# Kernel optimization log

Hardware: AMD Instinct MI355X
Metric: run time of the kernel (lower is better)

Reference implementation:

```python
import jax, jax.numpy as jnp
import numpy as np

B, N, D, H = 4, 2048, 768, 12
HD = D // H
SCALE = HD ** -0.5


def setup_inputs() -> dict:
    key = jax.random.key(0)
    k1, k2, k3 = jax.random.split(key, 3)
    x = jax.random.normal(k1, (B, N, D), dtype=jnp.float32)
    w_qkv = jax.random.normal(k2, (D, 3 * D), dtype=jnp.float32) * (D ** -0.5)
    w_proj = jax.random.normal(k3, (D, D), dtype=jnp.float32) * (D ** -0.5)
    b_proj = jnp.zeros((D,), dtype=jnp.float32)
    return {"x": x, "w_qkv": w_qkv, "w_proj": w_proj, "b_proj": b_proj}


def reference(x, w_qkv, w_proj, b_proj):
    b, n, d = x.shape
    qkv = x @ w_qkv                      # [b, n, 3d]
    q, k, v = jnp.split(qkv, 3, axis=-1)
    # [b, n, d] -> [b, h, n, hd]
    split_heads = lambda t: t.reshape(b, n, H, HD).transpose(0, 2, 1, 3)
    q, k, v = split_heads(q), split_heads(k), split_heads(v)
    dots = jnp.einsum('bhqd,bhkd->bhqk', q, k) * SCALE   # [b, h, n, n]
    attn = jax.nn.softmax(dots, axis=-1)
    q_attn = attn[:, :, 0, :]            # attention row of query token 0: [b, h, n]
    # dropout p=0 (eval) -> identity
    out = jnp.einsum('bhqk,bhkd->bhqd', attn, v)          # [b, h, n, hd]
    out = out.transpose(0, 2, 1, 3).reshape(b, n, d)      # [b, n, d]
    return out @ w_proj + b_proj, q_attn
```

## Files before the change

kernel.cpp:

```cpp
#include <hip/hip_runtime.h>


typedef unsigned short u16;
typedef __attribute__((ext_vector_type(8))) short bf8;
typedef __attribute__((ext_vector_type(4))) short bf4;
typedef __attribute__((ext_vector_type(4))) int i4;
typedef __attribute__((ext_vector_type(4))) float f4;

#define MFMA16(a, b, c) __builtin_amdgcn_mfma_f32_16x16x32_bf16((a), (b), (c), 0, 0, 0)

#if __has_builtin(__builtin_amdgcn_exp2f)
#define EXP2(x) __builtin_amdgcn_exp2f(x)
#else
#define EXP2(x) __expf((x) * 0.6931471805599453f)
#endif

__device__ __forceinline__ float b2f(u16 h) {
  union { unsigned u; float f; } v; v.u = ((unsigned)h) << 16; return v.f;
}
__device__ __forceinline__ u16 f2b(float f) {
  union { float f; unsigned u; } v; v.f = f;
  unsigned r = v.u + 0x7fffu + ((v.u >> 16) & 1u);
  return (u16)(r >> 16);
}
__device__ __forceinline__ unsigned pack2(float a, float b) {
#if __has_builtin(__builtin_amdgcn_perm)
  return __builtin_amdgcn_perm(__builtin_bit_cast(unsigned, b),
                               __builtin_bit_cast(unsigned, a), 0x07060302u);
#else
  return (__builtin_bit_cast(unsigned, b) & 0xFFFF0000u) |
         (__builtin_bit_cast(unsigned, a) >> 16);
#endif
}
__device__ __forceinline__ void gload16(const u16* g, u16* l) {
  __builtin_amdgcn_global_load_lds(
      (const __attribute__((address_space(1))) void*)g,
      (__attribute__((address_space(3))) void*)l, 16, 0, 0);
}
__device__ __forceinline__ int detect_f32(const u16* x) {
  unsigned v = x[2 * (threadIdx.x & 63)];
  unsigned e = (v >> 7) & 0xFF;
  return __ballot(e >= 0x8E) != 0ull;
}

__global__ __launch_bounds__(256) void prep(
    const void* __restrict__ x, u16* __restrict__ xbf,
    const void* __restrict__ wqkv, u16* __restrict__ wqkvT,
    const void* __restrict__ wproj, u16* __restrict__ wprojT) {
  const int z = blockIdx.z;
  if (z == 2) {
    const int f32 = detect_f32((const u16*)x);
    const int lin = blockIdx.y * 72 + blockIdx.x;
    if (f32) {
      const float2* in = (const float2*)x;
      unsigned* out = (unsigned*)xbf;
      for (int i = lin * 256 + threadIdx.x; i < 3145728; i += 442368) {
        float2 v = in[i];
        out[i] = (unsigned)f2b(v.x) | ((unsigned)f2b(v.y) << 16);
      }
    } else {
      const unsigned* in = (const unsigned*)x;
      unsigned* out = (unsigned*)xbf;
      for (int i = lin * 256 + threadIdx.x; i < 3145728; i += 442368)
        out[i] = in[i];
    }
    return;
  }
  if (z == 1 && blockIdx.x >= 24) return;
  const void* in = z ? wproj : wqkv;
  u16* out = z ? wprojT : wqkvT;
  const int R = 768, C = z ? 768 : 2304;
  __shared__ u16 tile[32][33];
  const int f32 = detect_f32((const u16*)x);
  const int bx = blockIdx.x * 32, by = blockIdx.y * 32;
  const int tx = threadIdx.x & 31, ty = threadIdx.x >> 5;
#pragma unroll
  for (int i = 0; i < 4; i++) {
    size_t idx = (size_t)(by + ty + i * 8) * C + bx + tx;
    tile[ty + i * 8][tx] = f32 ? f2b(((const float*)in)[idx]) : ((const u16*)in)[idx];
  }
  __syncthreads();
#pragma unroll
  for (int i = 0; i < 4; i++)
    out[(size_t)(bx + ty + i * 8) * R + by + tx] = tile[tx][ty + i * 8];
}

__global__ __launch_bounds__(512, 4) void gemm_qkv8(
    const u16* __restrict__ A, const u16* __restrict__ Bt,
    u16* __restrict__ Cq, u16* __restrict__ Vt) {
  __shared__ alignas(16) u16 L[3][13312];
  const int t = threadIdx.x;
  const int lane = t & 63, wave = t >> 6;
  const int wr = wave >> 1, wc = wave & 1;
  const int quad = lane >> 4, l16 = lane & 15;
  const int bm = blockIdx.y * 128, bn = blockIdx.x * 288;
  const int dcol = ((lane & 3) ^ ((lane >> 3) & 3)) * 8;
  const int swzU = (quad ^ ((l16 >> 1) & 3)) * 8;
  const int drow = lane >> 2;
  f4 acc[2][9] = {};

#define STAGE(kt, buf)                                                       \
  {                                                                          \
    _Pragma("unroll")                                                        \
    for (int s = 0; s < 4; s++) {                                            \
      int c = wave + s * 8;                                                  \
      if (c >= 26) c = wave;            \
      const int isB = c >= 8;                                                \
      const int rb = isB ? c - 8 : c;                                        \
      const u16* src = (isB ? Bt : A) +                                      \
          (size_t)((isB ? bn : bm) + rb * 16 + drow) * 768 +                 \
          (kt) * 32 + dcol;                                                  \
      u16* dst = &L[buf][(isB ? 4096 : 0) + rb * 512];                       \
      gload16(src, dst);                                                     \
    }                                                                        \
  }

  STAGE(0, 0);
  STAGE(1, 1);

  int cur = 0;
  for (int j = 0; j < 24; j++) {
    if (j < 23) {
      asm volatile("s_waitcnt vmcnt(4)" ::: "memory");
    } else {
      asm volatile("s_waitcnt vmcnt(0)" ::: "memory");
    }
    __builtin_amdgcn_s_barrier();
    if (j + 2 < 24) {
      int pre = cur + 2; if (pre >= 3) pre -= 3;
      STAGE(j + 2, pre);
    }
    const u16* Lb = &L[cur][0];
    bf8 af[2];
#pragma unroll
    for (int m = 0; m < 2; m++)
      af[m] = *(const bf8*)&Lb[(wr * 32 + m * 16 + l16) * 32 + swzU];
#pragma unroll
    for (int p = 0; p < 3; p++) {
      bf8 bfr[3];
#pragma unroll
      for (int nn = 0; nn < 3; nn++)
        bfr[nn] = *(const bf8*)&Lb[4096 +
            (wc * 144 + (p * 3 + nn) * 16 + l16) * 32 + swzU];
      __builtin_amdgcn_s_setprio(1);
#pragma unroll
      for (int nn = 0; nn < 3; nn++)
#pragma unroll
        for (int m = 0; m < 2; m++)
          acc[m][p * 3 + nn] = MFMA16(af[m], bfr[nn], acc[m][p * 3 + nn]);
      __builtin_amdgcn_s_setprio(0);
    }
    cur = (cur == 2) ? 0 : cur + 1;
  }
#undef STAGE

  const int b_ = bm >> 11;
#pragma unroll
  for (int m = 0; m < 2; m++) {
    const int row0 = bm + wr * 32 + m * 16 + quad * 4;
    const int n0 = row0 & 2047;
    const int n2 = (n0 & ~31) | (((n0 >> 2) & 3) << 3) | (((n0 >> 4) & 1) << 2);
#pragma unroll
    for (int ni = 0; ni < 9; ni++) {
      const int col = bn + wc * 144 + ni * 16 + l16;
      if (col >= 1536) {
        const int colv = col - 1536, h = colv >> 6, d = colv & 63;
        bf4 pk = {(short)f2b(acc[m][ni][0]), (short)f2b(acc[m][ni][1]),
                  (short)f2b(acc[m][ni][2]), (short)f2b(acc[m][ni][3])};
        *(bf4*)&Vt[(size_t)((b_ * 12 + h) * 64 + d) * 2048 + n2] = pk;
      } else {
#pragma unroll
        for (int r = 0; r < 4; r++)
          Cq[(size_t)(row0 + r) * 2304 + col] = f2b(acc[m][ni][r]);
      }
    }
  }
}

template <int BIAS, int QATTN>
__global__ __launch_bounds__(256, 4) void gemm_bt(
    const u16* __restrict__ A, const u16* __restrict__ Bt,
    const void* __restrict__ bias, void* __restrict__ C,
    int M, int Ncols, int K, const u16* __restrict__ xdet,
    u16* __restrict__ Vt, const float* __restrict__ qe,
    const float* __restrict__ lout) {
  if (QATTN && blockIdx.x == 6) {
    const int f32o = detect_f32(xdet);
    const int base = blockIdx.y * 1536;
    for (int j = threadIdx.x; j < 1536; j += 256) {
      int idx = base + j;
      float v = qe[idx] * (1.f / lout[idx >> 11]);
      size_t oidx = (size_t)6291456 + idx;
      if (f32o) ((float*)C)[oidx] = v; else ((u16*)C)[oidx] = f2b(v);
    }
    return;
  }
  __shared__ alignas(16) u16 Al[2][128 * 32];
  __shared__ alignas(16) u16 Bl[2][128 * 32];
  const int t = threadIdx.x;
  const int lane = t & 63, wave = t >> 6;
  const int wr = wave >> 1, wc = wave & 1;
  const int quad = lane >> 4, l16 = lane & 15;
  const int bm = blockIdx.y * 128, bn = blockIdx.x * 128;
  const int f32o = BIAS ? detect_f32(xdet) : 0;
  const int grow = lane >> 2, gcol = (lane & 3) * 8;
  const int chunk0 = wave * 2, chunk1 = wave * 2 + 1;
  const int arow0 = chunk0 * 16 + grow, arow1 = chunk1 * 16 + grow;
  f4 acc[4][4] = {};
  gload16(A + (size_t)(bm + arow0) * K + gcol, &Al[0][chunk0 * 512]);
  gload16(Bt + (size_t)(bn + arow0) * K + gcol, &Bl[0][chunk0 * 512]);
  gload16(A + (size_t)(bm + arow1) * K + gcol, &Al[0][chunk1 * 512]);
  gload16(Bt + (size_t)(bn + arow1) * K + gcol, &Bl[0][chunk1 * 512]);
  const int NIT = K >> 5;
  for (int i = 0; i < NIT; i++) {
    const int cur = i & 1, nxt = cur ^ 1;
    __syncthreads();
    if (i + 1 < NIT) {
      int k0 = (i + 1) << 5;
      gload16(A + (size_t)(bm + arow0) * K + k0 + gcol, &Al[nxt][chunk0 * 512]);
      gload16(Bt + (size_t)(bn + arow0) * K + k0 + gcol, &Bl[nxt][chunk0 * 512]);
      gload16(A + (size_t)(bm + arow1) * K + k0 + gcol, &Al[nxt][chunk1 * 512]);
      gload16(Bt + (size_t)(bn + arow1) * K + k0 + gcol, &Bl[nxt][chunk1 * 512]);
    }
    bf8 af[4], bfr[4];
#pragma unroll
    for (int mt = 0; mt < 4; mt++)
      af[mt] = *(const bf8*)&Al[cur][(wr * 64 + mt * 16 + l16) * 32 + quad * 8];
#pragma unroll
    for (int nt = 0; nt < 4; nt++)
      bfr[nt] = *(const bf8*)&Bl[cur][(wc * 64 + nt * 16 + l16) * 32 + quad * 8];
#pragma unroll
    for (int mt = 0; mt < 4; mt++)
#pragma unroll
      for (int nt = 0; nt < 4; nt++)
        acc[mt][nt] = MFMA16(af[mt], bfr[nt], acc[mt][nt]);
  }
  if (Vt != nullptr && bn >= 1536) {
    const int b = bm >> 11;
#pragma unroll
    for (int mt = 0; mt < 4; mt++) {
      int n0 = (bm & 2047) + wr * 64 + mt * 16 + quad * 4;
      int n2 = (n0 & ~31) | (((n0 >> 2) & 3) << 3) | (((n0 >> 4) & 1) << 2);
#pragma unroll
      for (int nt = 0; nt < 4; nt++) {
        int colv = bn - 1536 + wc * 64 + nt * 16 + l16;
        int h = colv >> 6, d = colv & 63;
        bf4 pk = {(short)f2b(acc[mt][nt][0]), (short)f2b(acc[mt][nt][1]),
                  (short)f2b(acc[mt][nt][2]), (short)f2b(acc[mt][nt][3])};
        *(bf4*)&Vt[(size_t)((b * 12 + h) * 64 + d) * 2048 + n2] = pk;
      }
    }
    return;
  }
#pragma unroll
  for (int mt = 0; mt < 4; mt++) {
    int row = bm + wr * 64 + mt * 16 + quad * 4;
#pragma unroll
    for (int nt = 0; nt < 4; nt++) {
      int col = bn + wc * 64 + nt * 16 + l16;
      float bv = 0.f;
      if (BIAS)
        bv = f32o ? ((const float*)bias)[col] : b2f(((const u16*)bias)[col]);
#pragma unroll
      for (int r = 0; r < 4; r++) {
        size_t idx = (size_t)(row + r) * Ncols + col;
        float v = acc[mt][nt][r] + bv;
        if (f32o) ((float*)C)[idx] = v; else ((u16*)C)[idx] = f2b(v);
      }
    }
  }
}

__global__ __launch_bounds__(256, 3) void flash_attn(
    const u16* __restrict__ qkv, const u16* __restrict__ Vt,
    u16* __restrict__ O, float* __restrict__ qe, float* __restrict__ lout) {
  __shared__ alignas(16) u16 lds[3][8192];
  const int t = threadIdx.x, lane = t & 63, wave = t >> 6;
  const int quad = lane >> 4, l16 = lane & 15;
  const int id = blockIdx.x;
  const int bh = (id & 7) + 8 * (id >> 7);
  const int qtile = (id >> 3) & 15;
  const int b = bh / 12, h = bh - b * 12;
  const int q0 = qtile * 128 + wave * 32;
  const bool dumpP = (qe != nullptr) && (qtile == 0) && (wave == 0);
  const float SCALE2 = 0.125f * 1.44269504089f;
  const float mM0 = -16.f;
  bf8 qf[2][2];
#pragma unroll
  for (int qt = 0; qt < 2; qt++) {
    const u16* Qr = qkv + (size_t)(b * 2048 + q0 + qt * 16 + l16) * 2304 + h * 64;
    bf8 r0 = *(const bf8*)(Qr + quad * 8);
    bf8 r1 = *(const bf8*)(Qr + 32 + quad * 8);
#pragma unroll
    for (int j = 0; j < 8; j++) {
      qf[qt][0][j] = (short)f2b(b2f((u16)r0[j]) * SCALE2);
      qf[qt][1][j] = (short)f2b(b2f((u16)r1[j]) * SCALE2);
    }
  }
  bf8 ones;
#pragma unroll
  for (int j = 0; j < 8; j++) ones[j] = (short)0x3F80;
  const u16* Kb = qkv + (size_t)(b * 2048) * 2304 + 768 + h * 64;
  const u16* Vb = Vt + (size_t)((b * 12 + h) * 64) * 2048;
  const int drow = wave * 16 + (lane >> 2);
  const int dcol = ((lane & 3) ^ ((lane >> 3) & 3)) * 8;
  const int swz = (quad ^ ((l16 >> 1) & 3)) * 8;
  f4 o[2][4] = {};
  f4 lacc[2] = {};

#define STAGE(tile, buf)                                            \
  {                                                                 \
    int n1_ = (tile) * 64;                                          \
    const u16* Kt_ = Kb + (size_t)(n1_ + drow) * 2304 + dcol;       \
    const u16* Vr_ = Vb + (size_t)drow * 2048 + n1_ + dcol;         \
    u16* base_ = &lds[buf][wave * 512];                             \
    gload16(Kt_, base_);                                            \
    gload16(Kt_ + 32, base_ + 2048);                                \
    gload16(Vr_, base_ + 4096);                                     \
    gload16(Vr_ + 32, base_ + 6144);                                \
  }

  STAGE(0, 0);
  STAGE(1, 1);

  int cur = 0;
  for (int i = 0; i < 32; i++) {
    if (i < 31) {
      asm volatile("s_waitcnt vmcnt(4)" ::: "memory");
    } else {
      asm volatile("s_waitcnt vmcnt(0)" ::: "memory");
    }
    __builtin_amdgcn_s_barrier();
    if (i + 2 < 32) {
      int pre = cur + 2; if (pre >= 3) pre -= 3;
      STAGE(i + 2, pre);
    }
    const u16* K0 = &lds[cur][0];
    const u16* K1 = &lds[cur][2048];
    union { i4 i; bf8 b; } pf[2][2];
#pragma unroll
    for (int kt = 0; kt < 4; kt++) {
      bf8 kf0 = *(const bf8*)&K0[(kt * 16 + l16) * 32 + swz];
      bf8 kf1 = *(const bf8*)&K1[(kt * 16 + l16) * 32 + swz];
#pragma unroll
      for (int qt = 0; qt < 2; qt++) {
        f4 z = {mM0, mM0, mM0, mM0};
        z = MFMA16(kf0, qf[qt][0], z);
        z = MFMA16(kf1, qf[qt][1], z);
        float e0 = EXP2(z[0]);
        float e1 = EXP2(z[1]);
        float e2 = EXP2(z[2]);
        float e3 = EXP2(z[3]);
        if (qt == 0 && dumpP && l16 == 0) {
          f4 ev = {e0, e1, e2, e3};
          *(f4*)&qe[bh * 2048 + i * 64 + kt * 16 + quad * 4] = ev;
        }
        pf[qt][kt >> 1].i[(kt & 1) * 2 + 0] = (int)pack2(e0, e1);
        pf[qt][kt >> 1].i[(kt & 1) * 2 + 1] = (int)pack2(e2, e3);
      }
    }
#pragma unroll
    for (int pair = 0; pair < 2; pair++) {
      const u16* Vp = &lds[cur][4096 + pair * 2048];
      lacc[0] = MFMA16(ones, pf[0][pair].b, lacc[0]);
      lacc[1] = MFMA16(ones, pf[1][pair].b, lacc[1]);
#pragma unroll
      for (int nt = 0; nt < 4; nt++) {
        bf8 vf = *(const bf8*)&Vp[(nt * 16 + l16) * 32 + swz];
        o[0][nt] = MFMA16(vf, pf[0][pair].b, o[0][nt]);
        o[1][nt] = MFMA16(vf, pf[1][pair].b, o[1][nt]);
      }
    }
    cur = (cur == 2) ? 0 : cur + 1;
  }
#undef STAGE
#pragma unroll
  for (int qt = 0; qt < 2; qt++) {
    float l = lacc[qt][0];
    if (qt == 0 && dumpP && lane == 0) lout[bh] = l;
    float inv = 1.f / l;
    size_t row = (size_t)(b * 2048 + q0 + qt * 16 + l16) * 768 + h * 64;
#pragma unroll
    for (int nt = 0; nt < 4; nt++) {
      bf4 pk = {(short)f2b(o[qt][nt][0] * inv), (short)f2b(o[qt][nt][1] * inv),
                (short)f2b(o[qt][nt][2] * inv), (short)f2b(o[qt][nt][3] * inv)};
      *(bf4*)&O[row + nt * 16 + quad * 4] = pk;
    }
  }
}

__global__ __launch_bounds__(256) void qattn_row0(
    const u16* __restrict__ qkv, void* __restrict__ out,
    const u16* __restrict__ xdet) {
  const int bh = blockIdx.x, b = bh / 12, h = bh % 12;
  __shared__ float qs[64];
  __shared__ float sv[2048];
  __shared__ float red[8];
  const int t = threadIdx.x;
  const int f32o = detect_f32(xdet);
  if (t < 64) qs[t] = b2f(qkv[(size_t)(b * 2048) * 2304 + h * 64 + t]);
  __syncthreads();
  float lmax = -1e30f;
  for (int k = t; k < 2048; k += 256) {
    const u16* Kr = qkv + (size_t)(b * 2048 + k) * 2304 + 768 + h * 64;
    float acc = 0.f;
#pragma unroll
    for (int j = 0; j < 8; j++) {
      bf8 kv = *(const bf8*)(Kr + j * 8);
#pragma unroll
      for (int d = 0; d < 8; d++) acc += qs[j * 8 + d] * b2f((u16)kv[d]);
    }
    acc *= 0.125f;
    sv[k] = acc;
    lmax = fmaxf(lmax, acc);
  }
#pragma unroll
  for (int off = 32; off >= 1; off >>= 1) lmax = fmaxf(lmax, __shfl_xor(lmax, off, 64));
  if ((t & 63) == 0) red[t >> 6] = lmax;
  __syncthreads();
  const float bmax = fmaxf(fmaxf(red[0], red[1]), fmaxf(red[2], red[3]));
  float lsum = 0.f;
  for (int k = t; k < 2048; k += 256) {
    float e = __expf(sv[k] - bmax);
    sv[k] = e;
    lsum += e;
  }
#pragma unroll
  for (int off = 32; off >= 1; off >>= 1) lsum += __shfl_xor(lsum, off, 64);
  if ((t & 63) == 0) red[4 + (t >> 6)] = lsum;
  __syncthreads();
  const float inv = 1.f / (red[4] + red[5] + red[6] + red[7]);
  for (int k = t; k < 2048; k += 256) {
    size_t idx = (size_t)6291456 + (size_t)bh * 2048 + k;
    float v = sv[k] * inv;
    if (f32o) ((float*)out)[idx] = v; else ((u16*)out)[idx] = f2b(v);
  }
}

extern "C" void kernel_launch(void* const* d_in, const int* in_sizes, int n_in,
                              void* d_out, int out_size, void* d_ws, size_t ws_size,
                              hipStream_t stream) {
  const void* x_raw      = d_in[0];
  const void* w_qkv_raw  = d_in[1];
  const void* w_proj_raw = d_in[2];
  const void* b_proj_raw = d_in[3];
  const u16* xdet = (const u16*)x_raw;
  char* ws = (char*)d_ws;
  u16* xbf    = (u16*)(ws + 256);
  u16* wqkvT  = (u16*)(ws + 12583168);
  u16* wprojT = (u16*)(ws + 16122112);
  u16* qkv    = (u16*)(ws + 17301760);
  u16* Vt     = (u16*)(ws + 55050496);
  float* qe   = (float*)(ws + 67633408);
  float* lout = (float*)(ws + 68026624);
  u16* attn   = xbf;
  const bool fused = ws_size >= 68026816ull;

  prep<<<dim3(72, 24, 3), 256, 0, stream>>>(
      x_raw, xbf, w_qkv_raw, wqkvT, w_proj_raw, wprojT);
  gemm_qkv8<<<dim3(8, 64), 512, 0, stream>>>(xbf, wqkvT, qkv, Vt);
  flash_attn<<<dim3(768), 256, 0, stream>>>(qkv, Vt, attn,
                                            fused ? qe : nullptr,
                                            fused ? lout : nullptr);
  if (fused) {
    gemm_bt<1, 1><<<dim3(7, 64), 256, 0, stream>>>(
        attn, wprojT, b_proj_raw, d_out, 8192, 768, 768, xdet, nullptr, qe, lout);
  } else {
    gemm_bt<1, 0><<<dim3(6, 64), 256, 0, stream>>>(
        attn, wprojT, b_proj_raw, d_out, 8192, 768, 768, xdet, nullptr, nullptr, nullptr);
    qattn_row0<<<dim3(48), 256, 0, stream>>>(qkv, d_out, xdet);
  }
}
```

Measured before the change: 209.1 us.

## Add dedicated projection GEMM with smaller tiles and triple-buffered async loads

New measurement: 208.2 us. No clear change (-0.4%).

```diff
diff --git a/kernel.cpp b/kernel.cpp
--- a/kernel.cpp
+++ b/kernel.cpp
@@ -172,6 +172,102 @@
 #pragma unroll
         for (int r = 0; r < 4; r++)
           Cq[(size_t)(row0 + r) * 2304 + col] = f2b(acc[m][ni][r]);
+      }
+    }
+  }
+}
+
+__global__ __launch_bounds__(256, 3) void gemm_proj4(
+    const u16* __restrict__ A, const u16* __restrict__ Bt,
+    const void* __restrict__ bias, void* __restrict__ C,
+    const u16* __restrict__ xdet, const float* __restrict__ qe,
+    const float* __restrict__ lout) {
+  if (blockIdx.x == 6) {
+    if (blockIdx.y >= 64) return;
+    const int f32o = detect_f32(xdet);
+    const int base = blockIdx.y * 1536;
+    for (int j = threadIdx.x; j < 1536; j += 256) {
+      int idx = base + j;
+      float v = qe[idx] * (1.f / lout[idx >> 11]);
+      size_t oidx = (size_t)6291456 + idx;
+      if (f32o) ((float*)C)[oidx] = v; else ((u16*)C)[oidx] = f2b(v);
+    }
+    return;
+  }
+  __shared__ alignas(16) u16 L[3][6144];
+  const int t = threadIdx.x;
+  const int lane = t & 63, wave = t >> 6;
+  const int wr = wave >> 1, wc = wave & 1;
+  const int quad = lane >> 4, l16 = lane & 15;
+  const int bm = blockIdx.y * 64, bn = blockIdx.x * 128;
+  const int f32o = detect_f32(xdet);
+  const int dcol = ((lane & 3) ^ ((lane >> 3) & 3)) * 8;
+  const int swzU = (quad ^ ((l16 >> 1) & 3)) * 8;
+  const int drow = lane >> 2;
+  f4 acc[2][4] = {};
+
+#define STAGE(kt, buf)                                                       \
+  {                                                                          \
+    _Pragma("unroll")                                                        \
+    for (int s = 0; s < 3; s++) {                                            \
+      const int c = wave + s * 4;                                            \
+      const int isB = c >= 4;                                                \
+      const int rb = isB ? c - 4 : c;                                        \
+      const u16* src = (isB ? Bt : A) +                                      \
+          (size_t)((isB ? bn : bm) + rb * 16 + drow) * 768 +                 \
+          (kt) * 32 + dcol;                                                  \
+      u16* dst = &L[buf][(isB ? 2048 : 0) + rb * 512];                       \
+      gload16(src, dst);                                                     \
+    }                                                                        \
+  }
+
+  STAGE(0, 0);
+  STAGE(1, 1);
+
+  int cur = 0;
+  for (int j = 0; j < 24; j++) {
+    if (j < 23) {
+      asm volatile("s_waitcnt vmcnt(3)" ::: "memory");
+    } else {
+      asm volatile("s_waitcnt vmcnt(0)" ::: "memory");
+    }
+    __builtin_amdgcn_s_barrier();
+    if (j + 2 < 24) {
+      int pre = cur + 2; if (pre >= 3) pre -= 3;
+      STAGE(j + 2, pre);
+    }
+    const u16* Lb = &L[cur][0];
+    bf8 af[2], bfr[4];
+#pragma unroll
+    for (int m = 0; m < 2; m++)
+      af[m] = *(const bf8*)&Lb[(wr * 32 + m * 16 + l16) * 32 + swzU];
+#pragma unroll
+    for (int nt = 0; nt < 4; nt++)
+      bfr[nt] = *(const bf8*)&Lb[2048 + (wc * 64 + nt * 16 + l16) * 32 + swzU];
+    __builtin_amdgcn_s_setprio(1);
+#pragma unroll
+    for (int nt = 0; nt < 4; nt++)
+#pragma unroll
+      for (int m = 0; m < 2; m++)
+        acc[m][nt] = MFMA16(af[m], bfr[nt], acc[m][nt]);
+    __builtin_amdgcn_s_setprio(0);
+    cur = (cur == 2) ? 0 : cur + 1;
+  }
+#undef STAGE
+
+#pragma unroll
+  for (int m = 0; m < 2; m++) {
+    const int row0 = bm + wr * 32 + m * 16 + quad * 4;
+#pragma unroll
+    for (int nt = 0; nt < 4; nt++) {
+      const int col = bn + wc * 64 + nt * 16 + l16;
+      const float bv = f32o ? ((const float*)bias)[col]
+                            : b2f(((const u16*)bias)[col]);
+#pragma unroll
+      for (int r = 0; r < 4; r++) {
+        size_t idx = (size_t)(row0 + r) * 768 + col;
+        float v = acc[m][nt][r] + bv;
+        if (f32o) ((float*)C)[idx] = v; else ((u16*)C)[idx] = f2b(v);
       }
     }
   }
@@ -463,8 +559,8 @@
                                             fused ? qe : nullptr,
                                             fused ? lout : nullptr);
   if (fused) {
-    gemm_bt<1, 1><<<dim3(7, 64), 256, 0, stream>>>(
-        attn, wprojT, b_proj_raw, d_out, 8192, 768, 768, xdet, nullptr, qe, lout);
+    gemm_proj4<<<dim3(7, 128), 256, 0, stream>>>(
+        attn, wprojT, b_proj_raw, d_out, xdet, qe, lout);
   } else {
     gemm_bt<1, 0><<<dim3(6, 64), 256, 0, stream>>>(
         attn, wprojT, b_proj_raw, d_out, 8192, 768, 768, xdet, nullptr, nullptr, nullptr);
```
